# Kernel tuning notes

Measured on AMD Instinct MI355X. Metric: run time of the kernel, lower is better.

## Reference

```python
import jax, jax.numpy as jnp
import numpy as np

WS = 25          # window_size
THRESHOLD = 3.5  # default threshold in find_low_quality_regions


def _conv1d_gelu(x, w, b, pad):
    # x: (N, C_in, L), w: (C_out, C_in, K) -> gelu(conv(x) + b), SAME length
    y = jax.lax.conv_general_dilated(
        x, w, window_strides=(1,), padding=[(pad, pad)],
        dimension_numbers=("NCH", "OIH", "NCH"))
    return jax.nn.gelu(y + b[None, :, None], approximate=False)


def setup_inputs() -> dict:
    key = jax.random.key(0)
    ks = jax.random.split(key, 12)
    B, T, D, H = 8, 25000, 256, 128
    s = 0.05
    return {
        "latents": jax.random.normal(ks[0], (B, T, D), jnp.float32),
        "conv0_w": jax.random.normal(ks[1], (H, D, 7), jnp.float32) * s,
        "conv0_b": jax.random.normal(ks[2], (H,), jnp.float32) * s,
        "conv1_w": jax.random.normal(ks[3], (H, H, 5), jnp.float32) * s,
        "conv1_b": jax.random.normal(ks[4], (H,), jnp.float32) * s,
        "conv2_w": jax.random.normal(ks[5], (H, H, 5), jnp.float32) * s,
        "conv2_b": jax.random.normal(ks[6], (H,), jnp.float32) * s,
        "head_w1": jax.random.normal(ks[7], (H, H), jnp.float32) * s,
        "head_b1": jax.random.normal(ks[8], (H,), jnp.float32) * s,
        "head_w2": jax.random.normal(ks[9], (1, H), jnp.float32) * s,
        "head_b2": jax.random.normal(ks[10], (1,), jnp.float32) * s,
    }


def reference(latents, conv0_w, conv0_b, conv1_w, conv1_b, conv2_w, conv2_b,
              head_w1, head_b1, head_w2, head_b2):
    B, T, D = latents.shape
    nw = (T - WS) // WS + 1  # number of non-overlapping windows
    # (B, nw, WS, D) -> (B*nw, D, WS): batch all windows through the critic
    x = latents[:, :nw * WS].reshape(B, nw, WS, D).reshape(B * nw, WS, D)
    x = jnp.transpose(x, (0, 2, 1))  # NCH
    x = _conv1d_gelu(x, conv0_w, conv0_b, pad=3)
    x = _conv1d_gelu(x, conv1_w, conv1_b, pad=2)
    x = _conv1d_gelu(x, conv2_w, conv2_b, pad=2)
    feat = x.mean(axis=2)  # AdaptiveAvgPool1d(1) -> (B*nw, H)
    h = jax.nn.gelu(feat @ head_w1.T + head_b1, approximate=False)
    score = jax.nn.sigmoid(h @ head_w2.T + head_b2)[:, 0] * 5.0  # (B*nw,)
    scores = score.reshape(B, nw).mean(axis=0)  # critic(window).mean() per window
    low_quality = scores < THRESHOLD  # windows the loop would append as regions
    return scores, low_quality
```

## Files before the change

kernel.cpp:

```cpp
#include <hip/hip_runtime.h>
#include <math.h>

#define BATCH 8
#define T_LEN 25000
#define NW    1000
#define WS    25
#define D0    256
#define H     128

typedef __bf16 bf16;
typedef bf16 bf16x8 __attribute__((ext_vector_type(8)));
typedef bf16 bf16x4 __attribute__((ext_vector_type(4)));
typedef float f32x4 __attribute__((ext_vector_type(4)));

__device__ __forceinline__ float gelu_fast(float x) {
    float y = 0.7978845608f * x * (1.0f + 0.044715f * x * x);
    float e = __expf(2.0f * y);
    float t = 1.0f - 2.0f * __builtin_amdgcn_rcpf(e + 1.0f);
    return 0.5f * x * (1.0f + t);
}

__global__ void repack_w(const float* __restrict__ w, bf16* __restrict__ dst,
                         int Cin, int K, int KSn, int total) {
    int t = blockIdx.x * 256 + threadIdx.x;
    if (t >= total) return;
    int j    = t & 7;
    int lane = (t >> 3) & 63;
    int mt   = (t >> 9) & 7;
    int ks   = (t >> 12) % KSn;
    int k    = t / (4096 * KSn);
    int m = lane & 15, q = lane >> 4;
    int co = mt * 16 + m;
    int ci = ks * 32 + q * 8 + j;
    dst[t] = (bf16)w[(co * Cin + ci) * K + k];
}

__global__ void cvt_bf16(const float* __restrict__ w, bf16* __restrict__ dst, int n) {
    int t = blockIdx.x * 256 + threadIdx.x;
    if (t < n) dst[t] = (bf16)w[t];
}

#define XT_LD 264
#define A_LD  136
#define OFF_A1   32736
#define OFF_FEAT 48512
#define OFF_H    49536
#define SMEM_BYTES 50560

__global__ __launch_bounds__(256, 3)
void critic_kernel(const float* __restrict__ lat,
                   const bf16* __restrict__ p0, const float* __restrict__ b0,
                   const bf16* __restrict__ p1, const float* __restrict__ b1,
                   const bf16* __restrict__ p2, const float* __restrict__ b2,
                   const bf16* __restrict__ hw1b, const float* __restrict__ hb1,
                   const float* __restrict__ hw2, const float* __restrict__ hb2,
                   float* __restrict__ scores_tmp) {
    __shared__ __align__(16) char smem[SMEM_BYTES];
    bf16  (*xT)[XT_LD]  = (bf16(*)[XT_LD])smem;
    bf16  (*a2T)[A_LD]  = (bf16(*)[A_LD])smem;
    bf16  (*a1T)[A_LD]  = (bf16(*)[A_LD])(smem + OFF_A1);
    float* feat = (float*)(smem + OFF_FEAT);
    float* hbuf = (float*)(smem + OFF_H);

    const int tid = threadIdx.x;
    const int bx  = blockIdx.x;
    const int b   = bx / (NW / 2);
    const int wi  = bx % (NW / 2);
    const int w0  = 2 * wi;

    {
        const float4* src4 = (const float4*)(lat + ((size_t)b * T_LEN + (size_t)w0 * WS) * D0);
        #pragma unroll
        for (int it = 0; it < 12; ++it) {
            int g = tid + it * 256;
            int l = g >> 6, c0 = (g & 63) * 4;
            int r = (l < 25) ? (l + 3) : (l + 9);
            float4 v = src4[g];
            bf16x4 o = {(bf16)v.x, (bf16)v.y, (bf16)v.z, (bf16)v.w};
            *(bf16x4*)&xT[r][c0] = o;
        }
        {
            if (tid < 128) {
                int g = 3072 + tid;
                int l = g >> 6, c0 = (g & 63) * 4;
                int r = (l < 25) ? (l + 3) : (l + 9);
                float4 v = src4[g];
                bf16x4 o = {(bf16)v.x, (bf16)v.y, (bf16)v.z, (bf16)v.w};
                *(bf16x4*)&xT[r][c0] = o;
            }
        }
        bf16x4 z4 = {};
        #pragma unroll
        for (int it = 0; it < 3; ++it) {
            int i = tid + it * 256;
            if (i < 768) {
                int rr = i >> 6;
                int r = (rr < 3) ? rr : ((rr < 9) ? rr + 25 : rr + 50);
                *(bf16x4*)&xT[r][(i & 63) * 4] = z4;
            }
        }
        if (tid < 256) {
            int rr = tid >> 5;
            int r = (rr < 2) ? rr : ((rr < 6) ? rr + 25 : rr + 50);
            *(bf16x4*)&a1T[r][(tid & 31) * 4] = z4;
        }
    }
    __syncthreads();

    const int lane = tid & 63, wv = tid >> 6;
    const int m = lane & 15, q = lane >> 4;
    const bf16* xb  = &xT[m][q * 8];
    const bf16* a1b = &a1T[m][q * 8];

    f32x4 acc[2][4] = {};
    {
        const bf16x8* A = (const bf16x8*)p0 + (size_t)wv * 64 + lane;
        #pragma unroll
        for (int k = 0; k < 7; ++k) {
            #pragma unroll
            for (int ks = 0; ks < 8; ++ks) {
                bf16x8 a0 = A[(k * 8 + ks) * 512];
                bf16x8 a1 = A[(k * 8 + ks) * 512 + 256];
                const bf16* pB = xb + k * XT_LD + ks * 32;
                bf16x8 bb0 = *(const bf16x8*)(pB);
                bf16x8 bb1 = *(const bf16x8*)(pB + 16 * XT_LD);
                bf16x8 bb2 = *(const bf16x8*)(pB + 31 * XT_LD);
                bf16x8 bb3 = *(const bf16x8*)(pB + 47 * XT_LD);
                acc[0][0] = __builtin_amdgcn_mfma_f32_16x16x32_bf16(a0, bb0, acc[0][0], 0, 0, 0);
                acc[0][1] = __builtin_amdgcn_mfma_f32_16x16x32_bf16(a0, bb1, acc[0][1], 0, 0, 0);
                acc[0][2] = __builtin_amdgcn_mfma_f32_16x16x32_bf16(a0, bb2, acc[0][2], 0, 0, 0);
                acc[0][3] = __builtin_amdgcn_mfma_f32_16x16x32_bf16(a0, bb3, acc[0][3], 0, 0, 0);
                acc[1][0] = __builtin_amdgcn_mfma_f32_16x16x32_bf16(a1, bb0, acc[1][0], 0, 0, 0);
                acc[1][1] = __builtin_amdgcn_mfma_f32_16x16x32_bf16(a1, bb1, acc[1][1], 0, 0, 0);
                acc[1][2] = __builtin_amdgcn_mfma_f32_16x16x32_bf16(a1, bb2, acc[1][2], 0, 0, 0);
                acc[1][3] = __builtin_amdgcn_mfma_f32_16x16x32_bf16(a1, bb3, acc[1][3], 0, 0, 0);
            }
        }
    }
    __syncthreads();
    {
        bf16x4 z4 = {};
        int rr = tid >> 5;
        int r = (rr < 2) ? rr : ((rr < 6) ? rr + 25 : rr + 50);
        *(bf16x4*)&a2T[r][(tid & 31) * 4] = z4;
    }
    #pragma unroll
    for (int mt = 0; mt < 2; ++mt) {
        int co0 = (wv + 4 * mt) * 16 + q * 4;
        f32x4 bv = *(const f32x4*)&b0[co0];
        #pragma unroll
        for (int nt = 0; nt < 4; ++nt) {
            int l = (nt & 1) * 16 + m;
            if (l < 25) {
                bf16x4 v;
                #pragma unroll
                for (int r = 0; r < 4; ++r)
                    v[r] = (bf16)gelu_fast(acc[mt][nt][r] + bv[r]);
                *(bf16x4*)&a1T[l + 2 + 29 * (nt >> 1)][co0] = v;
            }
        }
    }
    __syncthreads();

    f32x4 c1[2][4] = {};
    {
        const bf16x8* A = (const bf16x8*)p1 + (size_t)wv * 64 + lane;
        #pragma unroll
        for (int k = 0; k < 5; ++k) {
            #pragma unroll
            for (int ks = 0; ks < 4; ++ks) {
                bf16x8 a0 = A[(k * 4 + ks) * 512];
                bf16x8 a1 = A[(k * 4 + ks) * 512 + 256];
                const bf16* pB = a1b + k * A_LD + ks * 32;
                bf16x8 bb0 = *(const bf16x8*)(pB);
                bf16x8 bb1 = *(const bf16x8*)(pB + 16 * A_LD);
                bf16x8 bb2 = *(const bf16x8*)(pB + 29 * A_LD);
                bf16x8 bb3 = *(const bf16x8*)(pB + 45 * A_LD);
                c1[0][0] = __builtin_amdgcn_mfma_f32_16x16x32_bf16(a0, bb0, c1[0][0], 0, 0, 0);
                c1[0][1] = __builtin_amdgcn_mfma_f32_16x16x32_bf16(a0, bb1, c1[0][1], 0, 0, 0);
                c1[0][2] = __builtin_amdgcn_mfma_f32_16x16x32_bf16(a0, bb2, c1[0][2], 0, 0, 0);
                c1[0][3] = __builtin_amdgcn_mfma_f32_16x16x32_bf16(a0, bb3, c1[0][3], 0, 0, 0);
                c1[1][0] = __builtin_amdgcn_mfma_f32_16x16x32_bf16(a1, bb0, c1[1][0], 0, 0, 0);
                c1[1][1] = __builtin_amdgcn_mfma_f32_16x16x32_bf16(a1, bb1, c1[1][1], 0, 0, 0);
                c1[1][2] = __builtin_amdgcn_mfma_f32_16x16x32_bf16(a1, bb2, c1[1][2], 0, 0, 0);
                c1[1][3] = __builtin_amdgcn_mfma_f32_16x16x32_bf16(a1, bb3, c1[1][3], 0, 0, 0);
            }
        }
    }
    #pragma unroll
    for (int mt = 0; mt < 2; ++mt) {
        int co0 = (wv + 4 * mt) * 16 + q * 4;
        f32x4 bv = *(const f32x4*)&b1[co0];
        #pragma unroll
        for (int nt = 0; nt < 4; ++nt) {
            int l = (nt & 1) * 16 + m;
            if (l < 25) {
                bf16x4 v;
                #pragma unroll
                for (int r = 0; r < 4; ++r)
                    v[r] = (bf16)gelu_fast(c1[mt][nt][r] + bv[r]);
                *(bf16x4*)&a2T[l + 2 + 29 * (nt >> 1)][co0] = v;
            }
        }
    }
    __syncthreads();

    f32x4 c2[2][4] = {};
    {
        const bf16* a2b = &a2T[m][q * 8];
        const bf16x8* A = (const bf16x8*)p2 + (size_t)wv * 64 + lane;
        #pragma unroll
        for (int k = 0; k < 5; ++k) {
            #pragma unroll
            for (int ks = 0; ks < 4; ++ks) {
                bf16x8 a0 = A[(k * 4 + ks) * 512];
                bf16x8 a1 = A[(k * 4 + ks) * 512 + 256];
                const bf16* pB = a2b + k * A_LD + ks * 32;
                bf16x8 bb0 = *(const bf16x8*)(pB);
                bf16x8 bb1 = *(const bf16x8*)(pB + 16 * A_LD);
                bf16x8 bb2 = *(const bf16x8*)(pB + 29 * A_LD);
                bf16x8 bb3 = *(const bf16x8*)(pB + 45 * A_LD);
                c2[0][0] = __builtin_amdgcn_mfma_f32_16x16x32_bf16(a0, bb0, c2[0][0], 0, 0, 0);
                c2[0][1] = __builtin_amdgcn_mfma_f32_16x16x32_bf16(a0, bb1, c2[0][1], 0, 0, 0);
                c2[0][2] = __builtin_amdgcn_mfma_f32_16x16x32_bf16(a0, bb2, c2[0][2], 0, 0, 0);
                c2[0][3] = __builtin_amdgcn_mfma_f32_16x16x32_bf16(a0, bb3, c2[0][3], 0, 0, 0);
                c2[1][0] = __builtin_amdgcn_mfma_f32_16x16x32_bf16(a1, bb0, c2[1][0], 0, 0, 0);
                c2[1][1] = __builtin_amdgcn_mfma_f32_16x16x32_bf16(a1, bb1, c2[1][1], 0, 0, 0);
                c2[1][2] = __builtin_amdgcn_mfma_f32_16x16x32_bf16(a1, bb2, c2[1][2], 0, 0, 0);
                c2[1][3] = __builtin_amdgcn_mfma_f32_16x16x32_bf16(a1, bb3, c2[1][3], 0, 0, 0);
            }
        }
    }
    #pragma unroll
    for (int mt = 0; mt < 2; ++mt) {
        int co0 = (wv + 4 * mt) * 16 + q * 4;
        f32x4 bv = *(const f32x4*)&b2[co0];
        #pragma unroll
        for (int win = 0; win < 2; ++win) {
            f32x4 pool;
            #pragma unroll
            for (int r = 0; r < 4; ++r) {
                float s  = gelu_fast(c2[mt][2 * win][r] + bv[r]);
                float g1 = gelu_fast(c2[mt][2 * win + 1][r] + bv[r]);
                s += (m < 9) ? g1 : 0.0f;
                s += __shfl_xor(s, 1);
                s += __shfl_xor(s, 2);
                s += __shfl_xor(s, 4);
                s += __shfl_xor(s, 8);
                pool[r] = s * 0.04f;
            }
            if (m == 0) *(f32x4*)&feat[win * 128 + co0] = pool;
        }
    }
    __syncthreads();

    {
        int win = tid >> 7, co = tid & 127;
        const bf16x8* row = (const bf16x8*)(hw1b + co * H);
        const float* f = feat + win * 128;
        float a = hb1[co];
        #pragma unroll
        for (int jv = 0; jv < 16; ++jv) {
            bf16x8 w8 = row[jv];
            #pragma unroll
            for (int u = 0; u < 8; ++u)
                a += (float)w8[u] * f[jv * 8 + u];
        }
        hbuf[tid] = gelu_fast(a);
    }
    __syncthreads();

    if (tid < 128) {
        int win = tid >> 6, j = tid & 63;
        const float* hb = hbuf + win * 128;
        float p = hw2[j] * hb[j] + hw2[j + 64] * hb[j + 64];
        #pragma unroll
        for (int off = 32; off > 0; off >>= 1) p += __shfl_down(p, off);
        if (j == 0) {
            float z = p + hb2[0];
            scores_tmp[b * NW + w0 + win] = 5.0f / (1.0f + expf(-z));
        }
    }
}

__global__ void finalize_kernel(const float* __restrict__ tmp, float* __restrict__ out) {
    int w = blockIdx.x * 256 + threadIdx.x;
    if (w < NW) {
        float s = 0.0f;
        #pragma unroll
        for (int b = 0; b < BATCH; ++b) s += tmp[b * NW + w];
        s *= 0.125f;
        out[w] = s;
        out[NW + w] = (s < 3.5f) ? 1.0f : 0.0f;
    }
}

extern "C" void kernel_launch(void* const* d_in, const int* in_sizes, int n_in,
                              void* d_out, int out_size, void* d_ws, size_t ws_size,
                              hipStream_t stream) {
    const float* lat  = (const float*)d_in[0];
    const float* c0w  = (const float*)d_in[1];
    const float* c0b  = (const float*)d_in[2];
    const float* c1w  = (const float*)d_in[3];
    const float* c1b  = (const float*)d_in[4];
    const float* c2w  = (const float*)d_in[5];
    const float* c2b  = (const float*)d_in[6];
    const float* hw1  = (const float*)d_in[7];
    const float* hb1  = (const float*)d_in[8];
    const float* hw2  = (const float*)d_in[9];
    const float* hb2  = (const float*)d_in[10];

    bf16* p0   = (bf16*)d_ws;
    bf16* p1   = (bf16*)((char*)d_ws + 458752);
    bf16* p2   = (bf16*)((char*)d_ws + 622592);
    bf16* hw1b = (bf16*)((char*)d_ws + 786432);
    float* tmp = (float*)((char*)d_ws + 819200);

    const int n0 = 128 * 256 * 7;
    const int n1 = 128 * 128 * 5;
    repack_w<<<(n0 + 255) / 256, 256, 0, stream>>>(c0w, p0, 256, 7, 8, n0);
    repack_w<<<(n1 + 255) / 256, 256, 0, stream>>>(c1w, p1, 128, 5, 4, n1);
    repack_w<<<(n1 + 255) / 256, 256, 0, stream>>>(c2w, p2, 128, 5, 4, n1);
    cvt_bf16<<<64, 256, 0, stream>>>(hw1, hw1b, 128 * 128);

    critic_kernel<<<BATCH * (NW / 2), 256, 0, stream>>>(lat, p0, c0b, p1, c1b, p2, c2b,
                                                        hw1b, hb1, hw2, hb2, tmp);
    finalize_kernel<<<4, 256, 0, stream>>>(tmp, (float*)d_out);
}
```

Measured before the change: 504.5 us.

## Switch critic convs to 32x32x16 MFMA tiles, shrink LDS, fuse weight prep

Rewrites all three conv stages to use 32x32x16 bf16 MFMA, with each wave owning 32 output channels and two 32-row column tiles (one per window), and repacks the weights to match. LDS is reorganised so a1 overlays the input tile and a2 gets its own region, cutting shared memory enough to raise launch bounds to 4 blocks per CU. The four weight-prep launches are merged into a single prep kernel. In exchange, the larger accumulators raise register pressure and more padded columns (32 per window instead of 25) are computed.

```diff
diff --git a/kernel.cpp b/kernel.cpp
--- a/kernel.cpp
+++ b/kernel.cpp
@@ -12,6 +12,7 @@
 typedef bf16 bf16x8 __attribute__((ext_vector_type(8)));
 typedef bf16 bf16x4 __attribute__((ext_vector_type(4)));
 typedef float f32x4 __attribute__((ext_vector_type(4)));
+typedef float f32x16 __attribute__((ext_vector_type(16)));
 
 __device__ __forceinline__ float gelu_fast(float x) {
     float y = 0.7978845608f * x * (1.0f + 0.044715f * x * x);
@@ -20,34 +21,45 @@
     return 0.5f * x * (1.0f + t);
 }
 
-__global__ void repack_w(const float* __restrict__ w, bf16* __restrict__ dst,
-                         int Cin, int K, int KSn, int total) {
+__device__ __forceinline__ void repack_one(const float* __restrict__ w,
+                                           bf16* __restrict__ dst, int idx,
+                                           int Cin, int K, int KSn) {
+    int j    = idx & 7;
+    int lane = (idx >> 3) & 63;
+    int mt   = (idx >> 9) & 3;
+    int u    = idx >> 11;
+    int ks   = u % KSn;
+    int k    = u / KSn;
+    int co = mt * 32 + (lane & 31);
+    int ci = ks * 16 + (lane >> 5) * 8 + j;
+    dst[idx] = (bf16)w[(co * Cin + ci) * K + k];
+}
+
+__global__ void prep_kernel(const float* __restrict__ c0w, const float* __restrict__ c1w,
+                            const float* __restrict__ c2w, const float* __restrict__ hw1,
+                            bf16* __restrict__ p0, bf16* __restrict__ p1,
+                            bf16* __restrict__ p2, bf16* __restrict__ hw1b) {
     int t = blockIdx.x * 256 + threadIdx.x;
-    if (t >= total) return;
-    int j    = t & 7;
-    int lane = (t >> 3) & 63;
-    int mt   = (t >> 9) & 7;
-    int ks   = (t >> 12) % KSn;
-    int k    = t / (4096 * KSn);
-    int m = lane & 15, q = lane >> 4;
-    int co = mt * 16 + m;
-    int ci = ks * 32 + q * 8 + j;
-    dst[t] = (bf16)w[(co * Cin + ci) * K + k];
-}
-
-__global__ void cvt_bf16(const float* __restrict__ w, bf16* __restrict__ dst, int n) {
-    int t = blockIdx.x * 256 + threadIdx.x;
-    if (t < n) dst[t] = (bf16)w[t];
+    if (t < 229376) {
+        repack_one(c0w, p0, t, 256, 7, 16);
+    } else if (t < 311296) {
+        repack_one(c1w, p1, t - 229376, 128, 5, 8);
+    } else if (t < 393216) {
+        repack_one(c2w, p2, t - 311296, 128, 5, 8);
+    } else if (t < 409600) {
+        int i = t - 393216;
+        hw1b[i] = (bf16)hw1[i];
+    }
 }
 
 #define XT_LD 264
 #define A_LD  136
-#define OFF_A1   32736
-#define OFF_FEAT 48512
-#define OFF_H    49536
-#define SMEM_BYTES 50560
-
-__global__ __launch_bounds__(256, 3)
+#define OFF_A2   16384
+#define OFF_FEAT 34816
+#define OFF_H    35840
+#define SMEM_BYTES 36864
+
+__global__ __launch_bounds__(256, 4)
 void critic_kernel(const float* __restrict__ lat,
                    const bf16* __restrict__ p0, const float* __restrict__ b0,
                    const bf16* __restrict__ p1, const float* __restrict__ b1,
@@ -57,8 +69,8 @@
                    float* __restrict__ scores_tmp) {
     __shared__ __align__(16) char smem[SMEM_BYTES];
     bf16  (*xT)[XT_LD]  = (bf16(*)[XT_LD])smem;
-    bf16  (*a2T)[A_LD]  = (bf16(*)[A_LD])smem;
-    bf16  (*a1T)[A_LD]  = (bf16(*)[A_LD])(smem + OFF_A1);
+    bf16  (*a1T)[A_LD]  = (bf16(*)[A_LD])smem;
+    bf16  (*a2T)[A_LD]  = (bf16(*)[A_LD])(smem + OFF_A2);
     float* feat = (float*)(smem + OFF_FEAT);
     float* hbuf = (float*)(smem + OFF_H);
 
@@ -79,15 +91,13 @@
             bf16x4 o = {(bf16)v.x, (bf16)v.y, (bf16)v.z, (bf16)v.w};
             *(bf16x4*)&xT[r][c0] = o;
         }
-        {
-            if (tid < 128) {
-                int g = 3072 + tid;
-                int l = g >> 6, c0 = (g & 63) * 4;
-                int r = (l < 25) ? (l + 3) : (l + 9);
-                float4 v = src4[g];
-                bf16x4 o = {(bf16)v.x, (bf16)v.y, (bf16)v.z, (bf16)v.w};
-                *(bf16x4*)&xT[r][c0] = o;
-            }
+        if (tid < 128) {
+            int g = 3072 + tid;
+            int l = g >> 6, c0 = (g & 63) * 4;
+            int r = (l < 25) ? (l + 3) : (l + 9);
+            float4 v = src4[g];
+            bf16x4 o = {(bf16)v.x, (bf16)v.y, (bf16)v.z, (bf16)v.w};
+            *(bf16x4*)&xT[r][c0] = o;
         }
         bf16x4 z4 = {};
         #pragma unroll
@@ -99,157 +109,127 @@
                 *(bf16x4*)&xT[r][(i & 63) * 4] = z4;
             }
         }
-        if (tid < 256) {
-            int rr = tid >> 5;
+    }
+    __syncthreads();
+
+    const int lane = tid & 63, wv = tid >> 6;
+    const int n5 = lane & 31, q2 = lane >> 5;
+    const bf16* xb = &xT[n5][q2 * 8];
+
+    f32x16 accA = {}, accB = {};
+    {
+        const bf16x8* A = (const bf16x8*)p0 + (size_t)wv * 64 + lane;
+        #pragma unroll
+        for (int k = 0; k < 7; ++k) {
+            #pragma unroll
+            for (int ks = 0; ks < 16; ++ks) {
+                bf16x8 a = A[(k * 16 + ks) * 256];
+                bf16x8 bbA = *(const bf16x8*)(xb + k * XT_LD + ks * 16);
+                bf16x8 bbB = *(const bf16x8*)(xb + (k + 31) * XT_LD + ks * 16);
+                accA = __builtin_amdgcn_mfma_f32_32x32x16_bf16(a, bbA, accA, 0, 0, 0);
+                accB = __builtin_amdgcn_mfma_f32_32x32x16_bf16(a, bbB, accB, 0, 0, 0);
+            }
+        }
+    }
+    __syncthreads();
+    {
+        bf16x4 z4 = {};
+        #pragma unroll
+        for (int it = 0; it < 2; ++it) {
+            int i = tid + it * 256;
+            int rr = (i >> 5) & 7;
             int r = (rr < 2) ? rr : ((rr < 6) ? rr + 25 : rr + 50);
-            *(bf16x4*)&a1T[r][(tid & 31) * 4] = z4;
-        }
-    }
-    __syncthreads();
-
-    const int lane = tid & 63, wv = tid >> 6;
-    const int m = lane & 15, q = lane >> 4;
-    const bf16* xb  = &xT[m][q * 8];
-    const bf16* a1b = &a1T[m][q * 8];
-
-    f32x4 acc[2][4] = {};
-    {
-        const bf16x8* A = (const bf16x8*)p0 + (size_t)wv * 64 + lane;
-        #pragma unroll
-        for (int k = 0; k < 7; ++k) {
+            int c0 = (i & 31) * 4;
+            if (i < 256) *(bf16x4*)&a1T[r][c0] = z4;
+            else         *(bf16x4*)&a2T[r][c0] = z4;
+        }
+    }
+    #pragma unroll
+    for (int rq = 0; rq < 4; ++rq) {
+        int co0 = wv * 32 + 8 * rq + 4 * q2;
+        f32x4 bv = *(const f32x4*)&b0[co0];
+        if (n5 < 25) {
+            bf16x4 vA, vB;
+            #pragma unroll
+            for (int r = 0; r < 4; ++r) {
+                vA[r] = (bf16)gelu_fast(accA[4 * rq + r] + bv[r]);
+                vB[r] = (bf16)gelu_fast(accB[4 * rq + r] + bv[r]);
+            }
+            *(bf16x4*)&a1T[n5 + 2][co0] = vA;
+            *(bf16x4*)&a1T[n5 + 2 + 29][co0] = vB;
+        }
+    }
+    __syncthreads();
+
+    f32x16 c1A = {}, c1B = {};
+    {
+        const bf16* ab = &a1T[n5][q2 * 8];
+        const bf16x8* A = (const bf16x8*)p1 + (size_t)wv * 64 + lane;
+        #pragma unroll
+        for (int k = 0; k < 5; ++k) {
             #pragma unroll
             for (int ks = 0; ks < 8; ++ks) {
-                bf16x8 a0 = A[(k * 8 + ks) * 512];
-                bf16x8 a1 = A[(k * 8 + ks) * 512 + 256];
-                const bf16* pB = xb + k * XT_LD + ks * 32;
-                bf16x8 bb0 = *(const bf16x8*)(pB);
-                bf16x8 bb1 = *(const bf16x8*)(pB + 16 * XT_LD);
-                bf16x8 bb2 = *(const bf16x8*)(pB + 31 * XT_LD);
-                bf16x8 bb3 = *(const bf16x8*)(pB + 47 * XT_LD);
-                acc[0][0] = __builtin_amdgcn_mfma_f32_16x16x32_bf16(a0, bb0, acc[0][0], 0, 0, 0);
-                acc[0][1] = __builtin_amdgcn_mfma_f32_16x16x32_bf16(a0, bb1, acc[0][1], 0, 0, 0);
-                acc[0][2] = __builtin_amdgcn_mfma_f32_16x16x32_bf16(a0, bb2, acc[0][2], 0, 0, 0);
-                acc[0][3] = __builtin_amdgcn_mfma_f32_16x16x32_bf16(a0, bb3, acc[0][3], 0, 0, 0);
-                acc[1][0] = __builtin_amdgcn_mfma_f32_16x16x32_bf16(a1, bb0, acc[1][0], 0, 0, 0);
-                acc[1][1] = __builtin_amdgcn_mfma_f32_16x16x32_bf16(a1, bb1, acc[1][1], 0, 0, 0);
-                acc[1][2] = __builtin_amdgcn_mfma_f32_16x16x32_bf16(a1, bb2, acc[1][2], 0, 0, 0);
-                acc[1][3] = __builtin_amdgcn_mfma_f32_16x16x32_bf16(a1, bb3, acc[1][3], 0, 0, 0);
-            }
-        }
-    }
-    __syncthreads();
-    {
-        bf16x4 z4 = {};
-        int rr = tid >> 5;
-        int r = (rr < 2) ? rr : ((rr < 6) ? rr + 25 : rr + 50);
-        *(bf16x4*)&a2T[r][(tid & 31) * 4] = z4;
+                bf16x8 a = A[(k * 8 + ks) * 256];
+                bf16x8 bbA = *(const bf16x8*)(ab + k * A_LD + ks * 16);
+                bf16x8 bbB = *(const bf16x8*)(ab + (k + 29) * A_LD + ks * 16);
+                c1A = __builtin_amdgcn_mfma_f32_32x32x16_bf16(a, bbA, c1A, 0, 0, 0);
+                c1B = __builtin_amdgcn_mfma_f32_32x32x16_bf16(a, bbB, c1B, 0, 0, 0);
+            }
+        }
     }
     #pragma unroll
-    for (int mt = 0; mt < 2; ++mt) {
-        int co0 = (wv + 4 * mt) * 16 + q * 4;
-        f32x4 bv = *(const f32x4*)&b0[co0];
-        #pragma unroll
-        for (int nt = 0; nt < 4; ++nt) {
-            int l = (nt & 1) * 16 + m;
-            if (l < 25) {
-                bf16x4 v;
-                #pragma unroll
-                for (int r = 0; r < 4; ++r)
-                    v[r] = (bf16)gelu_fast(acc[mt][nt][r] + bv[r]);
-                *(bf16x4*)&a1T[l + 2 + 29 * (nt >> 1)][co0] = v;
-            }
-        }
-    }
-    __syncthreads();
-
-    f32x4 c1[2][4] = {};
-    {
-        const bf16x8* A = (const bf16x8*)p1 + (size_t)wv * 64 + lane;
+    for (int rq = 0; rq < 4; ++rq) {
+        int co0 = wv * 32 + 8 * rq + 4 * q2;
+        f32x4 bv = *(const f32x4*)&b1[co0];
+        if (n5 < 25) {
+            bf16x4 vA, vB;
+            #pragma unroll
+            for (int r = 0; r < 4; ++r) {
+                vA[r] = (bf16)gelu_fast(c1A[4 * rq + r] + bv[r]);
+                vB[r] = (bf16)gelu_fast(c1B[4 * rq + r] + bv[r]);
+            }
+            *(bf16x4*)&a2T[n5 + 2][co0] = vA;
+            *(bf16x4*)&a2T[n5 + 2 + 29][co0] = vB;
+        }
+    }
+    __syncthreads();
+
+    f32x16 c2A = {}, c2B = {};
+    {
+        const bf16* ab = &a2T[n5][q2 * 8];
+        const bf16x8* A = (const bf16x8*)p2 + (size_t)wv * 64 + lane;
         #pragma unroll
         for (int k = 0; k < 5; ++k) {
             #pragma unroll
-            for (int ks = 0; ks < 4; ++ks) {
-                bf16x8 a0 = A[(k * 4 + ks) * 512];
-                bf16x8 a1 = A[(k * 4 + ks) * 512 + 256];
-                const bf16* pB = a1b + k * A_LD + ks * 32;
-                bf16x8 bb0 = *(const bf16x8*)(pB);
-                bf16x8 bb1 = *(const bf16x8*)(pB + 16 * A_LD);
-                bf16x8 bb2 = *(const bf16x8*)(pB + 29 * A_LD);
-                bf16x8 bb3 = *(const bf16x8*)(pB + 45 * A_LD);
-                c1[0][0] = __builtin_amdgcn_mfma_f32_16x16x32_bf16(a0, bb0, c1[0][0], 0, 0, 0);
-                c1[0][1] = __builtin_amdgcn_mfma_f32_16x16x32_bf16(a0, bb1, c1[0][1], 0, 0, 0);
-                c1[0][2] = __builtin_amdgcn_mfma_f32_16x16x32_bf16(a0, bb2, c1[0][2], 0, 0, 0);
-                c1[0][3] = __builtin_amdgcn_mfma_f32_16x16x32_bf16(a0, bb3, c1[0][3], 0, 0, 0);
-                c1[1][0] = __builtin_amdgcn_mfma_f32_16x16x32_bf16(a1, bb0, c1[1][0], 0, 0, 0);
-                c1[1][1] = __builtin_amdgcn_mfma_f32_16x16x32_bf16(a1, bb1, c1[1][1], 0, 0, 0);
-                c1[1][2] = __builtin_amdgcn_mfma_f32_16x16x32_bf16(a1, bb2, c1[1][2], 0, 0, 0);
-                c1[1][3] = __builtin_amdgcn_mfma_f32_16x16x32_bf16(a1, bb3, c1[1][3], 0, 0, 0);
+            for (int ks = 0; ks < 8; ++ks) {
+                bf16x8 a = A[(k * 8 + ks) * 256];
+                bf16x8 bbA = *(const bf16x8*)(ab + k * A_LD + ks * 16);
+                bf16x8 bbB = *(const bf16x8*)(ab + (k + 29) * A_LD + ks * 16);
+                c2A = __builtin_amdgcn_mfma_f32_32x32x16_bf16(a, bbA, c2A, 0, 0, 0);
+                c2B = __builtin_amdgcn_mfma_f32_32x32x16_bf16(a, bbB, c2B, 0, 0, 0);
             }
         }
     }
     #pragma unroll
-    for (int mt = 0; mt < 2; ++mt) {
-        int co0 = (wv + 4 * mt) * 16 + q * 4;
-        f32x4 bv = *(const f32x4*)&b1[co0];
-        #pragma unroll
-        for (int nt = 0; nt < 4; ++nt) {
-            int l = (nt & 1) * 16 + m;
-            if (l < 25) {
-                bf16x4 v;
-                #pragma unroll
-                for (int r = 0; r < 4; ++r)
-                    v[r] = (bf16)gelu_fast(c1[mt][nt][r] + bv[r]);
-                *(bf16x4*)&a2T[l + 2 + 29 * (nt >> 1)][co0] = v;
-            }
-        }
-    }
-    __syncthreads();
-
-    f32x4 c2[2][4] = {};
-    {
-        const bf16* a2b = &a2T[m][q * 8];
-        const bf16x8* A = (const bf16x8*)p2 + (size_t)wv * 64 + lane;
-        #pragma unroll
-        for (int k = 0; k < 5; ++k) {
-            #pragma unroll
-            for (int ks = 0; ks < 4; ++ks) {
-                bf16x8 a0 = A[(k * 4 + ks) * 512];
-                bf16x8 a1 = A[(k * 4 + ks) * 512 + 256];
-                const bf16* pB = a2b + k * A_LD + ks * 32;
-                bf16x8 bb0 = *(const bf16x8*)(pB);
-                bf16x8 bb1 = *(const bf16x8*)(pB + 16 * A_LD);
-                bf16x8 bb2 = *(const bf16x8*)(pB + 29 * A_LD);
-                bf16x8 bb3 = *(const bf16x8*)(pB + 45 * A_LD);
-                c2[0][0] = __builtin_amdgcn_mfma_f32_16x16x32_bf16(a0, bb0, c2[0][0], 0, 0, 0);
-                c2[0][1] = __builtin_amdgcn_mfma_f32_16x16x32_bf16(a0, bb1, c2[0][1], 0, 0, 0);
-                c2[0][2] = __builtin_amdgcn_mfma_f32_16x16x32_bf16(a0, bb2, c2[0][2], 0, 0, 0);
-                c2[0][3] = __builtin_amdgcn_mfma_f32_16x16x32_bf16(a0, bb3, c2[0][3], 0, 0, 0);
-                c2[1][0] = __builtin_amdgcn_mfma_f32_16x16x32_bf16(a1, bb0, c2[1][0], 0, 0, 0);
-                c2[1][1] = __builtin_amdgcn_mfma_f32_16x16x32_bf16(a1, bb1, c2[1][1], 0, 0, 0);
-                c2[1][2] = __builtin_amdgcn_mfma_f32_16x16x32_bf16(a1, bb2, c2[1][2], 0, 0, 0);
-                c2[1][3] = __builtin_amdgcn_mfma_f32_16x16x32_bf16(a1, bb3, c2[1][3], 0, 0, 0);
-            }
-        }
-    }
-    #pragma unroll
-    for (int mt = 0; mt < 2; ++mt) {
-        int co0 = (wv + 4 * mt) * 16 + q * 4;
+    for (int rq = 0; rq < 4; ++rq) {
+        int co0 = wv * 32 + 8 * rq + 4 * q2;
         f32x4 bv = *(const f32x4*)&b2[co0];
-        #pragma unroll
-        for (int win = 0; win < 2; ++win) {
-            f32x4 pool;
-            #pragma unroll
-            for (int r = 0; r < 4; ++r) {
-                float s  = gelu_fast(c2[mt][2 * win][r] + bv[r]);
-                float g1 = gelu_fast(c2[mt][2 * win + 1][r] + bv[r]);
-                s += (m < 9) ? g1 : 0.0f;
-                s += __shfl_xor(s, 1);
-                s += __shfl_xor(s, 2);
-                s += __shfl_xor(s, 4);
-                s += __shfl_xor(s, 8);
-                pool[r] = s * 0.04f;
-            }
-            if (m == 0) *(f32x4*)&feat[win * 128 + co0] = pool;
+        f32x4 poolA, poolB;
+        #pragma unroll
+        for (int r = 0; r < 4; ++r) {
+            float sA = (n5 < 25) ? gelu_fast(c2A[4 * rq + r] + bv[r]) : 0.0f;
+            float sB = (n5 < 25) ? gelu_fast(c2B[4 * rq + r] + bv[r]) : 0.0f;
+            #pragma unroll
+            for (int off = 1; off < 32; off <<= 1) {
+                sA += __shfl_xor(sA, off);
+                sB += __shfl_xor(sB, off);
+            }
+            poolA[r] = sA * 0.04f;
+            poolB[r] = sB * 0.04f;
+        }
+        if (n5 == 0) {
+            *(f32x4*)&feat[co0] = poolA;
+            *(f32x4*)&feat[128 + co0] = poolB;
         }
     }
     __syncthreads();
@@ -316,13 +296,7 @@
     bf16* hw1b = (bf16*)((char*)d_ws + 786432);
     float* tmp = (float*)((char*)d_ws + 819200);
 
-    const int n0 = 128 * 256 * 7;
-    const int n1 = 128 * 128 * 5;
-    repack_w<<<(n0 + 255) / 256, 256, 0, stream>>>(c0w, p0, 256, 7, 8, n0);
-    repack_w<<<(n1 + 255) / 256, 256, 0, stream>>>(c1w, p1, 128, 5, 4, n1);
-    repack_w<<<(n1 + 255) / 256, 256, 0, stream>>>(c2w, p2, 128, 5, 4, n1);
-    cvt_bf16<<<64, 256, 0, stream>>>(hw1, hw1b, 128 * 128);
-
+    prep_kernel<<<1600, 256, 0, stream>>>(c0w, c1w, c2w, hw1, p0, p1, p2, hw1b);
     critic_kernel<<<BATCH * (NW / 2), 256, 0, stream>>>(lat, p0, c0b, p1, c1b, p2, c2b,
                                                         hw1b, hb1, hw2, hb2, tmp);
     finalize_kernel<<<4, 256, 0, stream>>>(tmp, (float*)d_out);
```

New measurement: 532.2 us. 1.06x slower.

## Process four windows per block to reuse weight fragments and fuse prep kernels

Applied to the files above, without the earlier changes.

Each block now handles four windows instead of two, so every weight fragment loaded from global memory feeds twice as many MFMAs. The shared-memory layout is reorganised: separate a1 and a2 buffers, larger padded input and feature regions. Launch bounds drop to two blocks per CU and the accumulator register count doubles. The four weight repack and convert launches are merged into one prep kernel to cut launch overhead. The cost is lower occupancy and higher register pressure.

```diff
diff --git a/kernel.cpp b/kernel.cpp
--- a/kernel.cpp
+++ b/kernel.cpp
@@ -20,34 +20,44 @@
     return 0.5f * x * (1.0f + t);
 }
 
-__global__ void repack_w(const float* __restrict__ w, bf16* __restrict__ dst,
-                         int Cin, int K, int KSn, int total) {
+__device__ __forceinline__ void repack_one(const float* __restrict__ w,
+                                           bf16* __restrict__ dst, int idx,
+                                           int Cin, int K, int KSn) {
+    int j    = idx & 7;
+    int lane = (idx >> 3) & 63;
+    int mt   = (idx >> 9) & 7;
+    int ks   = (idx >> 12) % KSn;
+    int k    = idx / (4096 * KSn);
+    int co = mt * 16 + (lane & 15);
+    int ci = ks * 32 + (lane >> 4) * 8 + j;
+    dst[idx] = (bf16)w[(co * Cin + ci) * K + k];
+}
+
+__global__ void prep_kernel(const float* __restrict__ c0w, const float* __restrict__ c1w,
+                            const float* __restrict__ c2w, const float* __restrict__ hw1,
+                            bf16* __restrict__ p0, bf16* __restrict__ p1,
+                            bf16* __restrict__ p2, bf16* __restrict__ hw1b) {
     int t = blockIdx.x * 256 + threadIdx.x;
-    if (t >= total) return;
-    int j    = t & 7;
-    int lane = (t >> 3) & 63;
-    int mt   = (t >> 9) & 7;
-    int ks   = (t >> 12) % KSn;
-    int k    = t / (4096 * KSn);
-    int m = lane & 15, q = lane >> 4;
-    int co = mt * 16 + m;
-    int ci = ks * 32 + q * 8 + j;
-    dst[t] = (bf16)w[(co * Cin + ci) * K + k];
-}
-
-__global__ void cvt_bf16(const float* __restrict__ w, bf16* __restrict__ dst, int n) {
-    int t = blockIdx.x * 256 + threadIdx.x;
-    if (t < n) dst[t] = (bf16)w[t];
+    if (t < 229376) {
+        repack_one(c0w, p0, t, 256, 7, 8);
+    } else if (t < 311296) {
+        repack_one(c1w, p1, t - 229376, 128, 5, 4);
+    } else if (t < 393216) {
+        repack_one(c2w, p2, t - 311296, 128, 5, 4);
+    } else if (t < 409600) {
+        int i = t - 393216;
+        hw1b[i] = (bf16)hw1[i];
+    }
 }
 
 #define XT_LD 264
 #define A_LD  136
-#define OFF_A1   32736
-#define OFF_FEAT 48512
-#define OFF_H    49536
-#define SMEM_BYTES 50560
-
-__global__ __launch_bounds__(256, 3)
+#define OFF_A2   33456
+#define OFF_FEAT 70752
+#define OFF_H    72800
+#define SMEM_BYTES 74848
+
+__global__ __launch_bounds__(256, 2)
 void critic_kernel(const float* __restrict__ lat,
                    const bf16* __restrict__ p0, const float* __restrict__ b0,
                    const bf16* __restrict__ p1, const float* __restrict__ b1,
@@ -57,52 +67,37 @@
                    float* __restrict__ scores_tmp) {
     __shared__ __align__(16) char smem[SMEM_BYTES];
     bf16  (*xT)[XT_LD]  = (bf16(*)[XT_LD])smem;
-    bf16  (*a2T)[A_LD]  = (bf16(*)[A_LD])smem;
-    bf16  (*a1T)[A_LD]  = (bf16(*)[A_LD])(smem + OFF_A1);
+    bf16  (*a1T)[A_LD]  = (bf16(*)[A_LD])smem;
+    bf16  (*a2T)[A_LD]  = (bf16(*)[A_LD])(smem + OFF_A2);
     float* feat = (float*)(smem + OFF_FEAT);
     float* hbuf = (float*)(smem + OFF_H);
 
     const int tid = threadIdx.x;
     const int bx  = blockIdx.x;
-    const int b   = bx / (NW / 2);
-    const int wi  = bx % (NW / 2);
-    const int w0  = 2 * wi;
+    const int b   = bx / (NW / 4);
+    const int wi  = bx % (NW / 4);
+    const int w0  = 4 * wi;
 
     {
         const float4* src4 = (const float4*)(lat + ((size_t)b * T_LEN + (size_t)w0 * WS) * D0);
         #pragma unroll
-        for (int it = 0; it < 12; ++it) {
+        for (int it = 0; it < 25; ++it) {
             int g = tid + it * 256;
             int l = g >> 6, c0 = (g & 63) * 4;
-            int r = (l < 25) ? (l + 3) : (l + 9);
+            int win = l / 25, lr = l - win * 25;
+            int r = 31 * win + lr + 3;
             float4 v = src4[g];
             bf16x4 o = {(bf16)v.x, (bf16)v.y, (bf16)v.z, (bf16)v.w};
             *(bf16x4*)&xT[r][c0] = o;
         }
-        {
-            if (tid < 128) {
-                int g = 3072 + tid;
-                int l = g >> 6, c0 = (g & 63) * 4;
-                int r = (l < 25) ? (l + 3) : (l + 9);
-                float4 v = src4[g];
-                bf16x4 o = {(bf16)v.x, (bf16)v.y, (bf16)v.z, (bf16)v.w};
-                *(bf16x4*)&xT[r][c0] = o;
-            }
-        }
         bf16x4 z4 = {};
         #pragma unroll
-        for (int it = 0; it < 3; ++it) {
+        for (int it = 0; it < 6; ++it) {
             int i = tid + it * 256;
-            if (i < 768) {
-                int rr = i >> 6;
-                int r = (rr < 3) ? rr : ((rr < 9) ? rr + 25 : rr + 50);
-                *(bf16x4*)&xT[r][(i & 63) * 4] = z4;
-            }
-        }
-        if (tid < 256) {
-            int rr = tid >> 5;
-            int r = (rr < 2) ? rr : ((rr < 6) ? rr + 25 : rr + 50);
-            *(bf16x4*)&a1T[r][(tid & 31) * 4] = z4;
+            int rr = i >> 6, c0 = (i & 63) * 4;
+            int j = rr / 6, t6 = rr - 6 * j;
+            int r = 31 * j + ((t6 < 3) ? t6 : t6 + 25);
+            *(bf16x4*)&xT[r][c0] = z4;
         }
     }
     __syncthreads();
@@ -112,7 +107,7 @@
     const bf16* xb  = &xT[m][q * 8];
     const bf16* a1b = &a1T[m][q * 8];
 
-    f32x4 acc[2][4] = {};
+    f32x4 acc[2][8] = {};
     {
         const bf16x8* A = (const bf16x8*)p0 + (size_t)wv * 64 + lane;
         #pragma unroll
@@ -121,48 +116,54 @@
             for (int ks = 0; ks < 8; ++ks) {
                 bf16x8 a0 = A[(k * 8 + ks) * 512];
                 bf16x8 a1 = A[(k * 8 + ks) * 512 + 256];
-                const bf16* pB = xb + k * XT_LD + ks * 32;
-                bf16x8 bb0 = *(const bf16x8*)(pB);
-                bf16x8 bb1 = *(const bf16x8*)(pB + 16 * XT_LD);
-                bf16x8 bb2 = *(const bf16x8*)(pB + 31 * XT_LD);
-                bf16x8 bb3 = *(const bf16x8*)(pB + 47 * XT_LD);
-                acc[0][0] = __builtin_amdgcn_mfma_f32_16x16x32_bf16(a0, bb0, acc[0][0], 0, 0, 0);
-                acc[0][1] = __builtin_amdgcn_mfma_f32_16x16x32_bf16(a0, bb1, acc[0][1], 0, 0, 0);
-                acc[0][2] = __builtin_amdgcn_mfma_f32_16x16x32_bf16(a0, bb2, acc[0][2], 0, 0, 0);
-                acc[0][3] = __builtin_amdgcn_mfma_f32_16x16x32_bf16(a0, bb3, acc[0][3], 0, 0, 0);
-                acc[1][0] = __builtin_amdgcn_mfma_f32_16x16x32_bf16(a1, bb0, acc[1][0], 0, 0, 0);
-                acc[1][1] = __builtin_amdgcn_mfma_f32_16x16x32_bf16(a1, bb1, acc[1][1], 0, 0, 0);
-                acc[1][2] = __builtin_amdgcn_mfma_f32_16x16x32_bf16(a1, bb2, acc[1][2], 0, 0, 0);
-                acc[1][3] = __builtin_amdgcn_mfma_f32_16x16x32_bf16(a1, bb3, acc[1][3], 0, 0, 0);
+                #pragma unroll
+                for (int win = 0; win < 4; ++win) {
+                    const bf16* pB = xb + (k + 31 * win) * XT_LD + ks * 32;
+                    bf16x8 bb0 = *(const bf16x8*)(pB);
+                    bf16x8 bb1 = *(const bf16x8*)(pB + 16 * XT_LD);
+                    acc[0][2 * win]     = __builtin_amdgcn_mfma_f32_16x16x32_bf16(a0, bb0, acc[0][2 * win], 0, 0, 0);
+                    acc[0][2 * win + 1] = __builtin_amdgcn_mfma_f32_16x16x32_bf16(a0, bb1, acc[0][2 * win + 1], 0, 0, 0);
+                    acc[1][2 * win]     = __builtin_amdgcn_mfma_f32_16x16x32_bf16(a1, bb0, acc[1][2 * win], 0, 0, 0);
+                    acc[1][2 * win + 1] = __builtin_amdgcn_mfma_f32_16x16x32_bf16(a1, bb1, acc[1][2 * win + 1], 0, 0, 0);
+                }
             }
         }
     }
     __syncthreads();
     {
         bf16x4 z4 = {};
-        int rr = tid >> 5;
-        int r = (rr < 2) ? rr : ((rr < 6) ? rr + 25 : rr + 50);
-        *(bf16x4*)&a2T[r][(tid & 31) * 4] = z4;
+        #pragma unroll
+        for (int it = 0; it < 4; ++it) {
+            int i = tid + it * 256;
+            int arr = i >> 9, rr = (i >> 5) & 15, c0 = (i & 31) * 4;
+            int j = rr >> 2, t4 = rr & 3;
+            int r = 29 * j + ((t4 < 2) ? t4 : t4 + 25);
+            if (arr == 0) *(bf16x4*)&a1T[r][c0] = z4;
+            else          *(bf16x4*)&a2T[r][c0] = z4;
+        }
     }
     #pragma unroll
     for (int mt = 0; mt < 2; ++mt) {
         int co0 = (wv + 4 * mt) * 16 + q * 4;
         f32x4 bv = *(const f32x4*)&b0[co0];
         #pragma unroll
-        for (int nt = 0; nt < 4; ++nt) {
-            int l = (nt & 1) * 16 + m;
-            if (l < 25) {
-                bf16x4 v;
-                #pragma unroll
-                for (int r = 0; r < 4; ++r)
-                    v[r] = (bf16)gelu_fast(acc[mt][nt][r] + bv[r]);
-                *(bf16x4*)&a1T[l + 2 + 29 * (nt >> 1)][co0] = v;
-            }
-        }
-    }
-    __syncthreads();
-
-    f32x4 c1[2][4] = {};
+        for (int win = 0; win < 4; ++win) {
+            #pragma unroll
+            for (int nt = 0; nt < 2; ++nt) {
+                int l = nt * 16 + m;
+                if (l < 25) {
+                    bf16x4 v;
+                    #pragma unroll
+                    for (int r = 0; r < 4; ++r)
+                        v[r] = (bf16)gelu_fast(acc[mt][2 * win + nt][r] + bv[r]);
+                    *(bf16x4*)&a1T[l + 2 + 29 * win][co0] = v;
+                }
+            }
+        }
+    }
+    __syncthreads();
+
+    f32x4 c1[2][8] = {};
     {
         const bf16x8* A = (const bf16x8*)p1 + (size_t)wv * 64 + lane;
         #pragma unroll
@@ -171,19 +172,16 @@
             for (int ks = 0; ks < 4; ++ks) {
                 bf16x8 a0 = A[(k * 4 + ks) * 512];
                 bf16x8 a1 = A[(k * 4 + ks) * 512 + 256];
-                const bf16* pB = a1b + k * A_LD + ks * 32;
-                bf16x8 bb0 = *(const bf16x8*)(pB);
-                bf16x8 bb1 = *(const bf16x8*)(pB + 16 * A_LD);
-                bf16x8 bb2 = *(const bf16x8*)(pB + 29 * A_LD);
-                bf16x8 bb3 = *(const bf16x8*)(pB + 45 * A_LD);
-                c1[0][0] = __builtin_amdgcn_mfma_f32_16x16x32_bf16(a0, bb0, c1[0][0], 0, 0, 0);
-                c1[0][1] = __builtin_amdgcn_mfma_f32_16x16x32_bf16(a0, bb1, c1[0][1], 0, 0, 0);
-                c1[0][2] = __builtin_amdgcn_mfma_f32_16x16x32_bf16(a0, bb2, c1[0][2], 0, 0, 0);
-                c1[0][3] = __builtin_amdgcn_mfma_f32_16x16x32_bf16(a0, bb3, c1[0][3], 0, 0, 0);
-                c1[1][0] = __builtin_amdgcn_mfma_f32_16x16x32_bf16(a1, bb0, c1[1][0], 0, 0, 0);
-                c1[1][1] = __builtin_amdgcn_mfma_f32_16x16x32_bf16(a1, bb1, c1[1][1], 0, 0, 0);
-                c1[1][2] = __builtin_amdgcn_mfma_f32_16x16x32_bf16(a1, bb2, c1[1][2], 0, 0, 0);
-                c1[1][3] = __builtin_amdgcn_mfma_f32_16x16x32_bf16(a1, bb3, c1[1][3], 0, 0, 0);
+                #pragma unroll
+                for (int win = 0; win < 4; ++win) {
+                    const bf16* pB = a1b + (k + 29 * win) * A_LD + ks * 32;
+                    bf16x8 bb0 = *(const bf16x8*)(pB);
+                    bf16x8 bb1 = *(const bf16x8*)(pB + 16 * A_LD);
+                    c1[0][2 * win]     = __builtin_amdgcn_mfma_f32_16x16x32_bf16(a0, bb0, c1[0][2 * win], 0, 0, 0);
+                    c1[0][2 * win + 1] = __builtin_amdgcn_mfma_f32_16x16x32_bf16(a0, bb1, c1[0][2 * win + 1], 0, 0, 0);
+                    c1[1][2 * win]     = __builtin_amdgcn_mfma_f32_16x16x32_bf16(a1, bb0, c1[1][2 * win], 0, 0, 0);
+                    c1[1][2 * win + 1] = __builtin_amdgcn_mfma_f32_16x16x32_bf16(a1, bb1, c1[1][2 * win + 1], 0, 0, 0);
+                }
             }
         }
     }
@@ -192,20 +190,23 @@
         int co0 = (wv + 4 * mt) * 16 + q * 4;
         f32x4 bv = *(const f32x4*)&b1[co0];
         #pragma unroll
-        for (int nt = 0; nt < 4; ++nt) {
-            int l = (nt & 1) * 16 + m;
-            if (l < 25) {
-                bf16x4 v;
-                #pragma unroll
-                for (int r = 0; r < 4; ++r)
-                    v[r] = (bf16)gelu_fast(c1[mt][nt][r] + bv[r]);
-                *(bf16x4*)&a2T[l + 2 + 29 * (nt >> 1)][co0] = v;
-            }
-        }
-    }
-    __syncthreads();
-
-    f32x4 c2[2][4] = {};
+        for (int win = 0; win < 4; ++win) {
+            #pragma unroll
+            for (int nt = 0; nt < 2; ++nt) {
+                int l = nt * 16 + m;
+                if (l < 25) {
+                    bf16x4 v;
+                    #pragma unroll
+                    for (int r = 0; r < 4; ++r)
+                        v[r] = (bf16)gelu_fast(c1[mt][2 * win + nt][r] + bv[r]);
+                    *(bf16x4*)&a2T[l + 2 + 29 * win][co0] = v;
+                }
+            }
+        }
+    }
+    __syncthreads();
+
+    f32x4 c2[2][8] = {};
     {
         const bf16* a2b = &a2T[m][q * 8];
         const bf16x8* A = (const bf16x8*)p2 + (size_t)wv * 64 + lane;
@@ -215,19 +216,16 @@
             for (int ks = 0; ks < 4; ++ks) {
                 bf16x8 a0 = A[(k * 4 + ks) * 512];
                 bf16x8 a1 = A[(k * 4 + ks) * 512 + 256];
-                const bf16* pB = a2b + k * A_LD + ks * 32;
-                bf16x8 bb0 = *(const bf16x8*)(pB);
-                bf16x8 bb1 = *(const bf16x8*)(pB + 16 * A_LD);
-                bf16x8 bb2 = *(const bf16x8*)(pB + 29 * A_LD);
-                bf16x8 bb3 = *(const bf16x8*)(pB + 45 * A_LD);
-                c2[0][0] = __builtin_amdgcn_mfma_f32_16x16x32_bf16(a0, bb0, c2[0][0], 0, 0, 0);
-                c2[0][1] = __builtin_amdgcn_mfma_f32_16x16x32_bf16(a0, bb1, c2[0][1], 0, 0, 0);
-                c2[0][2] = __builtin_amdgcn_mfma_f32_16x16x32_bf16(a0, bb2, c2[0][2], 0, 0, 0);
-                c2[0][3] = __builtin_amdgcn_mfma_f32_16x16x32_bf16(a0, bb3, c2[0][3], 0, 0, 0);
-                c2[1][0] = __builtin_amdgcn_mfma_f32_16x16x32_bf16(a1, bb0, c2[1][0], 0, 0, 0);
-                c2[1][1] = __builtin_amdgcn_mfma_f32_16x16x32_bf16(a1, bb1, c2[1][1], 0, 0, 0);
-                c2[1][2] = __builtin_amdgcn_mfma_f32_16x16x32_bf16(a1, bb2, c2[1][2], 0, 0, 0);
-                c2[1][3] = __builtin_amdgcn_mfma_f32_16x16x32_bf16(a1, bb3, c2[1][3], 0, 0, 0);
+                #pragma unroll
+                for (int win = 0; win < 4; ++win) {
+                    const bf16* pB = a2b + (k + 29 * win) * A_LD + ks * 32;
+                    bf16x8 bb0 = *(const bf16x8*)(pB);
+                    bf16x8 bb1 = *(const bf16x8*)(pB + 16 * A_LD);
+                    c2[0][2 * win]     = __builtin_amdgcn_mfma_f32_16x16x32_bf16(a0, bb0, c2[0][2 * win], 0, 0, 0);
+                    c2[0][2 * win + 1] = __builtin_amdgcn_mfma_f32_16x16x32_bf16(a0, bb1, c2[0][2 * win + 1], 0, 0, 0);
+                    c2[1][2 * win]     = __builtin_amdgcn_mfma_f32_16x16x32_bf16(a1, bb0, c2[1][2 * win], 0, 0, 0);
+                    c2[1][2 * win + 1] = __builtin_amdgcn_mfma_f32_16x16x32_bf16(a1, bb1, c2[1][2 * win + 1], 0, 0, 0);
+                }
             }
         }
     }
@@ -236,7 +234,7 @@
         int co0 = (wv + 4 * mt) * 16 + q * 4;
         f32x4 bv = *(const f32x4*)&b2[co0];
         #pragma unroll
-        for (int win = 0; win < 2; ++win) {
+        for (int win = 0; win < 4; ++win) {
             f32x4 pool;
             #pragma unroll
             for (int r = 0; r < 4; ++r) {
@@ -255,22 +253,27 @@
     __syncthreads();
 
     {
-        int win = tid >> 7, co = tid & 127;
+        int wb = tid >> 7, co = tid & 127;
         const bf16x8* row = (const bf16x8*)(hw1b + co * H);
-        const float* f = feat + win * 128;
-        float a = hb1[co];
+        const float* f0 = feat + wb * 128;
+        const float* f1 = feat + (wb + 2) * 128;
+        float a0h = hb1[co], a1h = a0h;
         #pragma unroll
         for (int jv = 0; jv < 16; ++jv) {
             bf16x8 w8 = row[jv];
             #pragma unroll
-            for (int u = 0; u < 8; ++u)
-                a += (float)w8[u] * f[jv * 8 + u];
-        }
-        hbuf[tid] = gelu_fast(a);
-    }
-    __syncthreads();
-
-    if (tid < 128) {
+            for (int u = 0; u < 8; ++u) {
+                float wf = (float)w8[u];
+                a0h += wf * f0[jv * 8 + u];
+                a1h += wf * f1[jv * 8 + u];
+            }
+        }
+        hbuf[wb * 128 + co] = gelu_fast(a0h);
+        hbuf[(wb + 2) * 128 + co] = gelu_fast(a1h);
+    }
+    __syncthreads();
+
+    {
         int win = tid >> 6, j = tid & 63;
         const float* hb = hbuf + win * 128;
         float p = hw2[j] * hb[j] + hw2[j + 64] * hb[j + 64];
@@ -316,14 +319,8 @@
     bf16* hw1b = (bf16*)((char*)d_ws + 786432);
     float* tmp = (float*)((char*)d_ws + 819200);
 
-    const int n0 = 128 * 256 * 7;
-    const int n1 = 128 * 128 * 5;
-    repack_w<<<(n0 + 255) / 256, 256, 0, stream>>>(c0w, p0, 256, 7, 8, n0);
-    repack_w<<<(n1 + 255) / 256, 256, 0, stream>>>(c1w, p1, 128, 5, 4, n1);
-    repack_w<<<(n1 + 255) / 256, 256, 0, stream>>>(c2w, p2, 128, 5, 4, n1);
-    cvt_bf16<<<64, 256, 0, stream>>>(hw1, hw1b, 128 * 128);
-
-    critic_kernel<<<BATCH * (NW / 2), 256, 0, stream>>>(lat, p0, c0b, p1, c1b, p2, c2b,
+    prep_kernel<<<1600, 256, 0, stream>>>(c0w, c1w, c2w, hw1, p0, p1, p2, hw1b);
+    critic_kernel<<<BATCH * (NW / 4), 256, 0, stream>>>(lat, p0, c0b, p1, c1b, p2, c2b,
                                                         hw1b, hb1, hw2, hb2, tmp);
     finalize_kernel<<<4, 256, 0, stream>>>(tmp, (float*)d_out);
 }
```

Result: faster. 464.9 us (-7.8%).
